# Kernel tuning notes

Hardware: AMD Instinct MI355X
Metric: run time of the kernel (lower is better)

The kernel has to match this reference:

```python
import jax, jax.numpy as jnp
import numpy as np

L = 8          # curve control points per chunk (self.l)
TS = 256       # curve spatial resolution (self.ts)


def setup_inputs() -> dict:
    key = jax.random.key(0)
    k1, k2 = jax.random.split(key)
    # full-resolution input image, values in [0,1)
    x = jax.random.uniform(k1, (4, 3, 1024, 1024), dtype=jnp.float32)
    # predicted curve parameters: 9*L = 72 channels at TS x TS
    param = jax.random.normal(k2, (4, 72, TS, TS), dtype=jnp.float32)
    return {"x": x, "param": param}


def _grid_sample_3d(vol, gx, gy, gz):
    """F.grid_sample(vol, grid, 'bilinear', 'border', align_corners=True)
    vol: [B,C,D,Hc,Wc]; gx,gy,gz: [B,H,W] normalized coords in [-1,1].
    Returns [B,H,W,C] (channels last)."""
    B, C, D, Hc, Wc = vol.shape
    # align_corners=True unnormalization + border padding (clamp coords)
    ix = jnp.clip((gx + 1.0) * 0.5 * (Wc - 1), 0.0, Wc - 1)
    iy = jnp.clip((gy + 1.0) * 0.5 * (Hc - 1), 0.0, Hc - 1)
    iz = jnp.clip((gz + 1.0) * 0.5 * (D - 1), 0.0, D - 1)
    x0f, y0f, z0f = jnp.floor(ix), jnp.floor(iy), jnp.floor(iz)
    wx, wy, wz = ix - x0f, iy - y0f, iz - z0f
    x0 = x0f.astype(jnp.int32); x1 = jnp.minimum(x0 + 1, Wc - 1)
    y0 = y0f.astype(jnp.int32); y1 = jnp.minimum(y0 + 1, Hc - 1)
    z0 = z0f.astype(jnp.int32); z1 = jnp.minimum(z0 + 1, D - 1)
    vol_t = vol.transpose(0, 2, 3, 4, 1)  # [B,D,Hc,Wc,C]
    b = jnp.arange(B)[:, None, None]      # [B,1,1]
    out = jnp.zeros(gx.shape + (C,), dtype=vol.dtype)
    for zi, wz_ in ((z0, 1.0 - wz), (z1, wz)):
        for yi, wy_ in ((y0, 1.0 - wy), (y1, wy)):
            for xi, wx_ in ((x0, 1.0 - wx), (x1, wx)):
                w = (wz_ * wy_ * wx_)[..., None]          # [B,H,W,1]
                out = out + w * vol_t[b, zi, yi, xi]      # gather -> [B,H,W,C]
    return out


def reference(x, param):
    # eval-mode forward of Generator.mapping + tanh (param precomputed by CNN)
    B, _, H, W = x.shape
    Hc, Wc = param.shape[-2], param.shape[-1]
    # torch.stack(torch.chunk(param,3,dim=1),dim=1) == reshape [B,3,3L,Hc,Wc]
    curve = param.reshape(B, 3, 3 * L, Hc, Wc)
    coordh = jnp.linspace(-1.0, 1.0, H, dtype=x.dtype)[:, None]  # varies over H
    coordw = jnp.linspace(-1.0, 1.0, W, dtype=x.dtype)[None, :]  # varies over W
    gx = jnp.broadcast_to(coordw, (B, H, W))
    gy = jnp.broadcast_to(coordh, (B, H, W))
    out = jnp.zeros((B, H, W, 3), dtype=x.dtype)
    for i in range(3):  # three curve chunks, z-coordinate = i-th color channel
        curve_i = curve[:, :, i * L:(i + 1) * L]          # [B,3,L,Hc,Wc]
        out = out + _grid_sample_3d(curve_i, gx, gy, x[:, i])
    return jnp.tanh(out.transpose(0, 3, 1, 2))            # [B,3,H,W]
```

## Files before the change

### kernel.cpp

```cpp
#include <hip/hip_runtime.h>
#include <math.h>

#define IMG 1024
#define HW (IMG * IMG)
#define TS 256
#define CH_STRIDE (TS * TS)
#define PARAM_B_STRIDE (72 * CH_STRIDE)
#define S_CONST (255.0f / 1023.0f)

#define ROWS 4
#define CELLS 34
#define CHS 45
#define CELL_DW 73
#define ROW_DW (CELLS * CELL_DW)
#define LDS_DW (ROWS * ROW_DW)
#define RUNS (ROWS * CHS)

__global__ __launch_bounds__(512, 8) void curve3d_fused(
    const float* __restrict__ x, const float* __restrict__ param,
    float* __restrict__ out)
{
    __shared__ float sh[LDS_DW];
    int blk = blockIdx.x;
    blk = (blk & 7) * 512 + (blk >> 3);
    int wt = blk & 7;
    int ht = (blk >> 3) & 127;
    int b  = blk >> 10;
    int tid = threadIdx.x;

    int w0 = wt * 128, h0 = ht * 8;
    int xb = (int)((float)w0 * S_CONST);
    int yb = (int)((float)h0 * S_CONST);

    int wx = tid & 15;
    int wyl = (tid >> 4) & 3;
    int pxp = tid >> 6;
    int tw = pxp * 16 + wx;
    int w = w0 + tw;
    int ha = h0 + wyl;

    const float* xp = x + (size_t)b * 3 * HW + (size_t)ha * IMG + w;
    float xv[2][3];
#pragma unroll
    for (int i = 0; i < 3; ++i) {
        xv[0][i] = __builtin_nontemporal_load(xp + (size_t)i * HW);
        xv[1][i] = __builtin_nontemporal_load(xp + (size_t)i * HW + 4 * IMG);
    }

    const float* pb = param + (size_t)b * PARAM_B_STRIDE;
    {
        int off = tid & 31;
        int cgrp = tid >> 5;
        int cc0 = cgrp, cc1 = 16 + cgrp, cc2 = 32 + cgrp;
        int cho0 = (cc0 / 5) * 8 + cc0 % 5 + 3;
        int cho1 = (cc1 / 5) * 8 + cc1 % 5 + 3;
        int cho2 = (cc2 / 5) * 8 + cc2 % 5 + 3;
        int vo0 = cho0 * CH_STRIDE + xb + off;
        int vo1 = cho1 * CH_STRIDE + xb + off;
        int vo2 = cho2 * CH_STRIDE + xb + off;
        int cb_ = off * CELL_DW;
        int lo0 = cb_ + (cho0 - 3);
        int lo1 = cb_ + (cho1 - 3);
        int lo2 = cb_ + (cho2 - 3);
        bool q2 = (cgrp < 13);
#pragma unroll
        for (int row = 0; row < ROWS; ++row) {
            int ys = min(yb + row, 255);
            const float* rb = pb + ys * TS;
            int rofs = row * ROW_DW;
            sh[rofs + lo0] = rb[vo0];
            sh[rofs + lo1] = rb[vo1];
            if (q2) sh[rofs + lo2] = rb[vo2];
        }
    }
    if (tid < 2 * RUNS) {
        int run = tid >> 1;
        int xx = 32 + (tid & 1);
        unsigned row = (unsigned)run / (unsigned)CHS;
        int chc = run - (int)row * CHS;
        int cho = (chc / 5) * 8 + chc % 5 + 3;
        int ys = min(yb + (int)row, 255);
        int xs = min(xb + xx, 255);
        sh[(int)row * ROW_DW + xx * CELL_DW + (cho - 3)] =
            pb[(size_t)cho * CH_STRIDE + ys * TS + xs];
    }

    int zo[2][3]; float wz[2][3];
#pragma unroll
    for (int p = 0; p < 2; ++p)
#pragma unroll
        for (int i = 0; i < 3; ++i) {
            float f = fminf(fmaxf(fmaf(xv[p][i], 3.5f, 3.5f), 0.0f), 7.0f);
            int z = min((int)f, 6);
            zo[p][i] = z - 3;
            wz[p][i] = f - (float)z;
        }

    float ixf = (float)w * S_CONST; int x0 = (int)ixf; float wxf = ixf - (float)x0;
    int cb0 = (x0 - xb) * CELL_DW;
    int cb1 = (min(x0 + 1, 255) - xb) * CELL_DW;
    float u0 = 1.0f - wxf;

    float wcs[2][4]; int bofs[2][4];
#pragma unroll
    for (int p = 0; p < 2; ++p) {
        int h = ha + p * 4;
        float iyf = (float)h * S_CONST; int y0 = (int)iyf; float wyf = iyf - (float)y0;
        int rb0 = (y0 - yb) * ROW_DW;
        int rb1 = (min(y0 + 1, 255) - yb) * ROW_DW;
        float v0 = 1.0f - wyf;
        wcs[p][0] = v0 * u0;  wcs[p][1] = v0 * wxf;
        wcs[p][2] = wyf * u0; wcs[p][3] = wyf * wxf;
        bofs[p][0] = rb0 + cb0; bofs[p][1] = rb0 + cb1;
        bofs[p][2] = rb1 + cb0; bofs[p][3] = rb1 + cb1;
    }

    __syncthreads();

    float acc[2][3] = {{0.0f, 0.0f, 0.0f}, {0.0f, 0.0f, 0.0f}};
#pragma unroll
    for (int i = 0; i < 3; ++i) {
#pragma unroll
        for (int k = 0; k < 4; ++k) {
#pragma unroll
            for (int p = 0; p < 2; ++p) {
                const float* bp = sh + bofs[p][k] + zo[p][i];
                float wk = wcs[p][k];
                float wzi = wz[p][i];
#pragma unroll
                for (int c = 0; c < 3; ++c) {
                    float2 v;
                    __builtin_memcpy(&v, bp + (c * 3 + i) * 8, 8);
                    float t = fmaf(wzi, v.y - v.x, v.x);
                    acc[p][c] = fmaf(wk, t, acc[p][c]);
                }
            }
        }
    }

    float* op = out + (size_t)b * 3 * HW + (size_t)ha * IMG + w;
#pragma unroll
    for (int p = 0; p < 2; ++p) {
        float* opp = op + (size_t)(p * 4) * IMG;
#pragma unroll
        for (int c = 0; c < 3; ++c) {
            float e = __expf(2.0f * acc[p][c]);
            opp[(size_t)c * HW] = 1.0f - 2.0f / (e + 1.0f);
        }
    }
}

extern "C" void kernel_launch(void* const* d_in, const int* in_sizes, int n_in,
                              void* d_out, int out_size, void* d_ws, size_t ws_size,
                              hipStream_t stream) {
    const float* x = (const float*)d_in[0];
    const float* param = (const float*)d_in[1];
    float* out = (float*)d_out;
    curve3d_fused<<<dim3(4 * 128 * 8), dim3(512), 0, stream>>>(x, param, out);
}
```

Baseline: 175.9 us.

## Shrink tiles to 64x4 pixels with 256-thread blocks, split z-lerp weights

Each block now covers a 64x4 pixel tile with one pixel per thread instead of a 128x8 tile with two pixels per thread. The block count quadruples and the LDS footprint per block shrinks to 3 rows by 18 cells, with a padded row stride. The z-interpolation is folded into two separate weights so each sample needs two FMAs into paired accumulators instead of a subtract plus two FMAs. The compute phase is wrapped in s_setprio. The trade-off is more redundant param loads per output pixel from overlapping halo rows and columns, plus more block launch overhead.

```diff
diff --git a/kernel.cpp b/kernel.cpp
--- a/kernel.cpp
+++ b/kernel.cpp
@@ -8,27 +8,27 @@
 #define PARAM_B_STRIDE (72 * CH_STRIDE)
 #define S_CONST (255.0f / 1023.0f)
 
-#define ROWS 4
-#define CELLS 34
+#define ROWS 3
+#define CELLS 18
 #define CHS 45
 #define CELL_DW 73
-#define ROW_DW (CELLS * CELL_DW)
+#define ROW_DW 1330
 #define LDS_DW (ROWS * ROW_DW)
-#define RUNS (ROWS * CHS)
+#define TAILN (ROWS * CHS * 2)
 
-__global__ __launch_bounds__(512, 8) void curve3d_fused(
+__global__ __launch_bounds__(256, 8) void curve3d_fused(
     const float* __restrict__ x, const float* __restrict__ param,
     float* __restrict__ out)
 {
     __shared__ float sh[LDS_DW];
     int blk = blockIdx.x;
-    blk = (blk & 7) * 512 + (blk >> 3);
-    int wt = blk & 7;
-    int ht = (blk >> 3) & 127;
-    int b  = blk >> 10;
+    blk = (blk & 7) * 2048 + (blk >> 3);
+    int wt = blk & 15;
+    int ht = (blk >> 4) & 255;
+    int b  = blk >> 12;
     int tid = threadIdx.x;
 
-    int w0 = wt * 128, h0 = ht * 8;
+    int w0 = wt * 64, h0 = ht * 4;
     int xb = (int)((float)w0 * S_CONST);
     int yb = (int)((float)h0 * S_CONST);
 
@@ -37,20 +37,18 @@
     int pxp = tid >> 6;
     int tw = pxp * 16 + wx;
     int w = w0 + tw;
-    int ha = h0 + wyl;
+    int h = h0 + wyl;
 
-    const float* xp = x + (size_t)b * 3 * HW + (size_t)ha * IMG + w;
-    float xv[2][3];
+    const float* xp = x + (size_t)b * 3 * HW + (size_t)h * IMG + w;
+    float xv[3];
 #pragma unroll
-    for (int i = 0; i < 3; ++i) {
-        xv[0][i] = __builtin_nontemporal_load(xp + (size_t)i * HW);
-        xv[1][i] = __builtin_nontemporal_load(xp + (size_t)i * HW + 4 * IMG);
-    }
+    for (int i = 0; i < 3; ++i)
+        xv[i] = __builtin_nontemporal_load(xp + (size_t)i * HW);
 
     const float* pb = param + (size_t)b * PARAM_B_STRIDE;
     {
-        int off = tid & 31;
-        int cgrp = tid >> 5;
+        int off = tid & 15;
+        int cgrp = tid >> 4;
         int cc0 = cgrp, cc1 = 16 + cgrp, cc2 = 32 + cgrp;
         int cho0 = (cc0 / 5) * 8 + cc0 % 5 + 3;
         int cho1 = (cc1 / 5) * 8 + cc1 % 5 + 3;
@@ -73,80 +71,74 @@
             if (q2) sh[rofs + lo2] = rb[vo2];
         }
     }
-    if (tid < 2 * RUNS) {
-        int run = tid >> 1;
-        int xx = 32 + (tid & 1);
-        unsigned row = (unsigned)run / (unsigned)CHS;
-        int chc = run - (int)row * CHS;
-        int cho = (chc / 5) * 8 + chc % 5 + 3;
-        int ys = min(yb + (int)row, 255);
-        int xs = min(xb + xx, 255);
-        sh[(int)row * ROW_DW + xx * CELL_DW + (cho - 3)] =
-            pb[(size_t)cho * CH_STRIDE + ys * TS + xs];
+    {
+#pragma unroll
+        for (int t = 0; t < 2; ++t) {
+            int run = tid + t * 256;
+            if (run < TAILN) {
+                unsigned row = (unsigned)run / (unsigned)(CHS * 2);
+                int rem = run - (int)row * (CHS * 2);
+                int xx = 16 + (rem >= CHS ? 1 : 0);
+                int chc = rem - (rem >= CHS ? CHS : 0);
+                int cho = (chc / 5) * 8 + chc % 5 + 3;
+                int ys = min(yb + (int)row, 255);
+                int xs = min(xb + xx, 255);
+                sh[(int)row * ROW_DW + xx * CELL_DW + (cho - 3)] =
+                    pb[(size_t)cho * CH_STRIDE + ys * TS + xs];
+            }
+        }
     }
 
-    int zo[2][3]; float wz[2][3];
+    int zo[3]; float wz[3];
 #pragma unroll
-    for (int p = 0; p < 2; ++p)
-#pragma unroll
-        for (int i = 0; i < 3; ++i) {
-            float f = fminf(fmaxf(fmaf(xv[p][i], 3.5f, 3.5f), 0.0f), 7.0f);
-            int z = min((int)f, 6);
-            zo[p][i] = z - 3;
-            wz[p][i] = f - (float)z;
-        }
+    for (int i = 0; i < 3; ++i) {
+        float f = fminf(fmaxf(fmaf(xv[i], 3.5f, 3.5f), 0.0f), 7.0f);
+        int z = min((int)f, 6);
+        zo[i] = z - 3;
+        wz[i] = f - (float)z;
+    }
 
     float ixf = (float)w * S_CONST; int x0 = (int)ixf; float wxf = ixf - (float)x0;
     int cb0 = (x0 - xb) * CELL_DW;
     int cb1 = (min(x0 + 1, 255) - xb) * CELL_DW;
     float u0 = 1.0f - wxf;
-
-    float wcs[2][4]; int bofs[2][4];
-#pragma unroll
-    for (int p = 0; p < 2; ++p) {
-        int h = ha + p * 4;
-        float iyf = (float)h * S_CONST; int y0 = (int)iyf; float wyf = iyf - (float)y0;
-        int rb0 = (y0 - yb) * ROW_DW;
-        int rb1 = (min(y0 + 1, 255) - yb) * ROW_DW;
-        float v0 = 1.0f - wyf;
-        wcs[p][0] = v0 * u0;  wcs[p][1] = v0 * wxf;
-        wcs[p][2] = wyf * u0; wcs[p][3] = wyf * wxf;
-        bofs[p][0] = rb0 + cb0; bofs[p][1] = rb0 + cb1;
-        bofs[p][2] = rb1 + cb0; bofs[p][3] = rb1 + cb1;
-    }
+    float iyf = (float)h * S_CONST; int y0 = (int)iyf; float wyf = iyf - (float)y0;
+    int rb0 = (y0 - yb) * ROW_DW;
+    int rb1 = (min(y0 + 1, 255) - yb) * ROW_DW;
+    float v0 = 1.0f - wyf;
+    float wcs[4] = {v0 * u0, v0 * wxf, wyf * u0, wyf * wxf};
+    int bofs[4] = {rb0 + cb0, rb0 + cb1, rb1 + cb0, rb1 + cb1};
 
     __syncthreads();
 
-    float acc[2][3] = {{0.0f, 0.0f, 0.0f}, {0.0f, 0.0f, 0.0f}};
+    __builtin_amdgcn_s_setprio(1);
+    float2 acc2[3] = {{0.f, 0.f}, {0.f, 0.f}, {0.f, 0.f}};
 #pragma unroll
     for (int i = 0; i < 3; ++i) {
+        float wzi = wz[i];
+        int zoi = zo[i];
 #pragma unroll
         for (int k = 0; k < 4; ++k) {
+            const float* bp = sh + bofs[k] + zoi;
+            float wb = wcs[k] * wzi;
+            float wa = wcs[k] - wb;
 #pragma unroll
-            for (int p = 0; p < 2; ++p) {
-                const float* bp = sh + bofs[p][k] + zo[p][i];
-                float wk = wcs[p][k];
-                float wzi = wz[p][i];
-#pragma unroll
-                for (int c = 0; c < 3; ++c) {
-                    float2 v;
-                    __builtin_memcpy(&v, bp + (c * 3 + i) * 8, 8);
-                    float t = fmaf(wzi, v.y - v.x, v.x);
-                    acc[p][c] = fmaf(wk, t, acc[p][c]);
-                }
+            for (int c = 0; c < 3; ++c) {
+                float2 v;
+                __builtin_memcpy(&v, bp + (c * 3 + i) * 8, 8);
+                acc2[c].x = fmaf(wa, v.x, acc2[c].x);
+                acc2[c].y = fmaf(wb, v.y, acc2[c].y);
             }
         }
     }
+    __builtin_amdgcn_s_setprio(0);
 
-    float* op = out + (size_t)b * 3 * HW + (size_t)ha * IMG + w;
+    float* op = out + (size_t)b * 3 * HW + (size_t)h * IMG + w;
 #pragma unroll
-    for (int p = 0; p < 2; ++p) {
-        float* opp = op + (size_t)(p * 4) * IMG;
-#pragma unroll
-        for (int c = 0; c < 3; ++c) {
-            float e = __expf(2.0f * acc[p][c]);
-            opp[(size_t)c * HW] = 1.0f - 2.0f / (e + 1.0f);
-        }
+    for (int c = 0; c < 3; ++c) {
+        float a = acc2[c].x + acc2[c].y;
+        float e = __expf(2.0f * a);
+        op[(size_t)c * HW] = 1.0f - 2.0f / (e + 1.0f);
     }
 }
 
@@ -156,5 +148,5 @@
     const float* x = (const float*)d_in[0];
     const float* param = (const float*)d_in[1];
     float* out = (float*)d_out;
-    curve3d_fused<<<dim3(4 * 128 * 8), dim3(512), 0, stream>>>(x, param, out);
+    curve3d_fused<<<dim3(4 * 256 * 16), dim3(256), 0, stream>>>(x, param, out);
 }
```

Measured after the change: 186.6 us. +6.0%, slower.
